# Optimization experiments

Hardware: AMD Instinct MI355X
Metric: run time of the kernel (lower is better)

The kernel has to match this reference:

```python
import jax, jax.numpy as jnp
import numpy as np
import math

N_HEAD = 12
BLOCK = 256  # local attention block size (ls)
EPS = 1e-6


def _rotate(x):
    # pairs (a, b) -> (-b, a) over last dim (matches rotate_embeddings)
    a = x[..., 0::2]
    b = x[..., 1::2]
    return jnp.stack([-b, a], axis=-1).reshape(x.shape)


def setup_inputs() -> dict:
    key = jax.random.key(0)
    k1, k2, k3 = jax.random.split(key, 3)
    B, T, C = 4, 8192, 768
    s = 0.02
    return {
        "x": jax.random.normal(k1, (B, T, C), jnp.float32),
        "w_qkv": jax.random.normal(k2, (C, 3 * C), jnp.float32) * s,
        "w_ln": jnp.ones((C,), jnp.float32),
        "w_proj": jax.random.normal(k3, (C, C), jnp.float32) * s,
    }


def reference(x, w_qkv, w_ln, w_proj):
    B, T, C = x.shape
    nh, ls = N_HEAD, BLOCK
    hd = C // nh
    ng = T // ls

    xb = x.reshape(B, ng, ls, C)
    qkv = xb @ w_qkv                                   # (B,ng,ls,3C)
    q, k, v = jnp.split(qkv, 3, axis=-1)

    # QK RMSNorm over full embedding dim (before head split)
    def rms(t):
        return t * jax.lax.rsqrt(jnp.mean(t * t, axis=-1, keepdims=True) + EPS) * w_ln
    q, k = rms(q), rms(k)

    # split heads: (B,ng,nh,ls,hd)
    def heads(t):
        return jnp.swapaxes(t.reshape(B, ng, ls, nh, hd), 2, 3)
    q, k, v = heads(q), heads(k), heads(v)

    # RoPE (repo layout: freqs tiled via cat((ts,ts)), interleaved pair rotation)
    pos = 10000.0 ** ((-2.0 * jnp.arange(0, hd, 2, dtype=jnp.float32) - 1.0) / hd)
    ts = jnp.arange(ls, dtype=jnp.float32)[:, None] * pos[None, :]   # (ls, hd/2)
    rot = jnp.concatenate([ts, ts], axis=-1)                          # (ls, hd)
    cos, sin = jnp.cos(rot), jnp.sin(rot)
    q = q * cos + _rotate(q) * sin
    k = k * cos + _rotate(k) * sin

    # block-causal scores: causal only within each local block
    scale = 1.0 / math.sqrt(hd)
    att = jnp.einsum('bgnqd,bgnkd->bgnqk', q, k) * scale              # (B,ng,nh,ls,ls)
    mask = jnp.tril(jnp.ones((ls, ls), dtype=bool))
    att = jnp.where(mask, att, -jnp.finfo(att.dtype).max)
    att = jax.nn.softmax(att, axis=-1)
    y = jnp.einsum('bgnqk,bgnkd->bgnqd', att, v)                      # (B,ng,nh,ls,hd)

    y = jnp.swapaxes(y, 2, 3).reshape(B, ng, ls, C)
    y = y @ w_proj
    return y.reshape(B, T, C)
```

## Files before the change

kernel.cpp:

```cpp
#include <hip/hip_runtime.h>
#include <math.h>

typedef __attribute__((ext_vector_type(8))) short bf16x8;
typedef __attribute__((ext_vector_type(4))) short bf16x4;
typedef __attribute__((ext_vector_type(2))) short bf16x2;
typedef __attribute__((ext_vector_type(4))) float f32x4;
typedef __attribute__((ext_vector_type(16))) float f32x16;

#define NH 12
#define HD 64
#define C0 768
#define C3 2304
#define LS 256
#define KT12 12

static __device__ __forceinline__ float bf2f(short u) {
  union { unsigned int i; float f; } c;
  c.i = ((unsigned int)(unsigned short)u) << 16;
  return c.f;
}
static __device__ __forceinline__ short f2bf(float f) {
  union { float f; unsigned int i; } c; c.f = f;
  unsigned int x = c.i;
  x += 0x7fffu + ((x >> 16) & 1u);
  return (short)(x >> 16);
}
static __device__ __forceinline__ unsigned pk2(float a, float b) {
  return (unsigned)(unsigned short)f2bf(a) | ((unsigned)(unsigned short)f2bf(b) << 16);
}

static __device__ __forceinline__ void gload_lds16(const short* g, const short* l) {
  unsigned long long ga = (unsigned long long)g;
  unsigned int la = (unsigned int)(unsigned long long)l;
  __builtin_amdgcn_global_load_lds(
      (const __attribute__((address_space(1))) void*)ga,
      (__attribute__((address_space(3))) void*)la, 16, 0, 0);
}

__global__ __launch_bounds__(256) void cast_pack_A_kernel(const float* __restrict__ x,
                                                          short* __restrict__ Apk) {
  __shared__ short sb[256 * 64];
  int bm = blockIdx.x, kt = blockIdx.y, t = threadIdx.x;
#pragma unroll
  for (int i = 0; i < 8; ++i) {
    int seg = i * 256 + t;
    int row = seg >> 3, sc8 = seg & 7;
    const float* src = x + ((long)(bm * 256 + row)) * C0 + kt * 64 + sc8 * 8;
    float4 v0 = *(const float4*)src;
    float4 v1 = *(const float4*)(src + 4);
    bf16x8 o = { f2bf(v0.x), f2bf(v0.y), f2bf(v0.z), f2bf(v0.w),
                 f2bf(v1.x), f2bf(v1.y), f2bf(v1.z), f2bf(v1.w) };
    *(bf16x8*)&sb[row * 64 + ((sc8 ^ (row & 7)) << 3)] = o;
  }
  __syncthreads();
#pragma unroll
  for (int i = 0; i < 8; ++i) {
    int c = i * 256 + t;
    int l = c & 63, f = c >> 6;
    int ks = f & 3, mt = (f >> 2) & 3, mh = f >> 4;
    int row = mh * 128 + mt * 32 + (l & 31);
    int kc = ks * 2 + (l >> 5);
    bf16x8 v = *(bf16x8*)&sb[row * 64 + ((kc ^ (row & 7)) << 3)];
    *(bf16x8*)&Apk[(((long)bm * KT12 + kt) * 2048 + c) * 8] = v;
  }
}

template <int WNG>
__global__ __launch_bounds__(256) void cast_pack_B_kernel(const float* __restrict__ w,
                                                          short* __restrict__ Bpk, int N) {
  __shared__ short sb[WNG * 64 * 64];
  int bn = blockIdx.x, kt = blockIdx.y, t = threadIdx.x;
#pragma unroll
  for (int i = 0; i < WNG * 2; ++i) {
    int seg = i * 256 + t;
    int k = seg / (WNG * 8);
    int nc = (seg % (WNG * 8)) * 8;
    const float* src = w + ((long)(kt * 64 + k)) * N + bn * (WNG * 64) + nc;
    float4 v0 = *(const float4*)src;
    float4 v1 = *(const float4*)(src + 4);
    sb[(nc + 0) * 64 + k] = f2bf(v0.x); sb[(nc + 1) * 64 + k] = f2bf(v0.y);
    sb[(nc + 2) * 64 + k] = f2bf(v0.z); sb[(nc + 3) * 64 + k] = f2bf(v0.w);
    sb[(nc + 4) * 64 + k] = f2bf(v1.x); sb[(nc + 5) * 64 + k] = f2bf(v1.y);
    sb[(nc + 6) * 64 + k] = f2bf(v1.z); sb[(nc + 7) * 64 + k] = f2bf(v1.w);
  }
  __syncthreads();
#pragma unroll
  for (int i = 0; i < WNG * 2; ++i) {
    int c = i * 256 + t;
    int l = c & 63, f = c >> 6;
    int ks = f & 3, nt = (f >> 2) & 1, wng = f >> 3;
    int col = wng * 64 + nt * 32 + (l & 31);
    int kk = ks * 16 + (l >> 5) * 8;
    bf16x8 v = *(bf16x8*)&sb[col * 64 + kk];
    *(bf16x8*)&Bpk[(((long)bn * KT12 + kt) * (WNG * 512) + c) * 8] = v;
  }
}

__global__ void rope_tab_kernel(float* __restrict__ cost, float* __restrict__ sint) {
  int t = blockIdx.x, d = threadIdx.x;
  int i = d & 31;
  float freq = powf(10000.0f, -(float)(4 * i + 1) / 64.0f);
  float th = (float)t * freq;
  cost[t * 64 + d] = cosf(th);
  sint[t * 64 + d] = sinf(th);
}

#define PH_OPEN                                        \
  __builtin_amdgcn_s_barrier();                        \
  asm volatile("s_waitcnt lgkmcnt(0)" ::: "memory");   \
  __builtin_amdgcn_sched_barrier(0);                   \
  __builtin_amdgcn_s_setprio(1);
#define PH_MID __builtin_amdgcn_s_setprio(0);
#define PH_CLOSE                                       \
  asm volatile("s_waitcnt vmcnt(2)" ::: "memory");     \
  __builtin_amdgcn_s_barrier();
#define MM8(ASET, BSET, MP, NT)                                                     \
  { _Pragma("unroll") for (int m2_ = 0; m2_ < 2; ++m2_)                             \
      _Pragma("unroll") for (int ks_ = 0; ks_ < 4; ++ks_)                           \
        acc[(MP)*2 + m2_][NT] = __builtin_amdgcn_mfma_f32_32x32x16_bf16(            \
            ASET[m2_ * 4 + ks_], BSET[ks_], acc[(MP)*2 + m2_][NT], 0, 0, 0); }

template <int OUT_F32>
__global__ __launch_bounds__(512, 2) void gemm32_kernel(const short* __restrict__ Apk,
                                                        const short* __restrict__ Bpk,
                                                        void* __restrict__ Cout,
                                                        int N, int K, int nbn) {
  __shared__ short lds[65536];
  int t = threadIdx.x, lane = t & 63, wave = t >> 6;
  int wm = (wave >> 2) * 128, wng = wave & 3, wn = wng * 64, mh = wave >> 2;
  int id = blockIdx.x;
  int cpx = gridDim.x >> 3;
  int sw = (id & 7) * cpx + (id >> 3);
  int bm = sw / nbn, bn = sw % nbn;

  f32x16 acc[4][2];
#pragma unroll
  for (int m = 0; m < 4; ++m)
#pragma unroll
    for (int n = 0; n < 2; ++n)
#pragma unroll
      for (int r = 0; r < 16; ++r) acc[m][n][r] = 0.f;

  bf16x8 a0[8], a1[8], b0[4], b1[4];

  auto STAGE = [&](int s) {
    if (s >= 4 * KT12) return;
    int q = s & 3, Ts = s >> 2;
    int bb = (Ts & 1) * 32768;
    if (q < 2) {
      int c = q * 1024 + t;
      const short* src = Apk + ((long)bm * KT12 + Ts) * 16384 + (long)c * 8;
      gload_lds16(src, &lds[bb + c * 8]);
      gload_lds16(src + 4096, &lds[bb + (c + 512) * 8]);
    } else {
      int c = (q - 2) * 1024 + t;
      const short* src = Bpk + ((long)bn * KT12 + Ts) * 16384 + (long)c * 8;
      gload_lds16(src, &lds[bb + 16384 + c * 8]);
      gload_lds16(src + 4096, &lds[bb + 16384 + (c + 512) * 8]);
    }
  };
  auto LDA = [&](bf16x8* d, int b, int mhalf) {
#pragma unroll
    for (int m2 = 0; m2 < 2; ++m2)
#pragma unroll
      for (int ks = 0; ks < 4; ++ks)
        d[m2 * 4 + ks] =
            *(bf16x8*)&lds[b * 32768 + ((mh * 16 + (mhalf * 2 + m2) * 4 + ks) * 64 + lane) * 8];
  };
  auto LDB = [&](bf16x8* d, int b, int nt) {
#pragma unroll
    for (int ks = 0; ks < 4; ++ks)
      d[ks] = *(bf16x8*)&lds[b * 32768 + 16384 + ((wng * 8 + nt * 4 + ks) * 64 + lane) * 8];
  };

  for (int s = 0; s < 7; ++s) STAGE(s);
  asm volatile("s_waitcnt vmcnt(6)" ::: "memory");
  __builtin_amdgcn_s_barrier();
  LDA(a0, 0, 0);
  LDB(b0, 0, 0);
  LDB(b1, 0, 1);

  for (int it = 0; it < KT12 / 2; ++it) {
    int P0 = 8 * it;
    PH_OPEN; MM8(a0, b0, 0, 0); PH_MID;
    LDA(a1, 0, 1); STAGE(P0 + 7); PH_CLOSE;
    PH_OPEN; MM8(a0, b1, 0, 1); PH_MID;
    LDA(a0, 1, 0); STAGE(P0 + 8); PH_CLOSE;
    PH_OPEN; MM8(a1, b0, 1, 0); PH_MID;
    LDB(b0, 1, 0); STAGE(P0 + 9); PH_CLOSE;
    PH_OPEN; MM8(a1, b1, 1, 1); PH_MID;
    LDB(b1, 1, 1); STAGE(P0 + 10); PH_CLOSE;
    PH_OPEN; MM8(a0, b0, 0, 0); PH_MID;
    LDA(a1, 1, 1); STAGE(P0 + 11); PH_CLOSE;
    PH_OPEN; MM8(a0, b1, 0, 1); PH_MID;
    LDA(a0, 0, 0); STAGE(P0 + 12); PH_CLOSE;
    PH_OPEN; MM8(a1, b0, 1, 0); PH_MID;
    LDB(b0, 0, 0); STAGE(P0 + 13); PH_CLOSE;
    PH_OPEN; MM8(a1, b1, 1, 1); PH_MID;
    LDB(b1, 0, 1); STAGE(P0 + 14); PH_CLOSE;
  }

  long crow0 = (long)bm * 256 + wm;
  long ccol0 = (long)bn * 256 + wn;
  int rbase = 4 * (lane >> 5);
  int cl = lane & 31;
#pragma unroll
  for (int mt = 0; mt < 4; ++mt)
#pragma unroll
    for (int nt = 0; nt < 2; ++nt)
#pragma unroll
      for (int reg = 0; reg < 16; ++reg) {
        long row = crow0 + mt * 32 + (reg & 3) + 8 * (reg >> 2) + rbase;
        long col = ccol0 + nt * 32 + cl;
        float v = acc[mt][nt][reg];
        if (OUT_F32) ((float*)Cout)[row * N + col] = v;
        else ((short*)Cout)[row * N + col] = f2bf(v);
      }
}

template <int OUT_F32>
__global__ __launch_bounds__(256, 2) void gemm128_kernel(const short* __restrict__ Arm,
                                                         const short* __restrict__ Bpk,
                                                         void* __restrict__ Cout,
                                                         int N, int K, int nbn) {
  __shared__ short lds[32768];
  int t = threadIdx.x, lane = t & 63, wave = t >> 6;
  int wm = (wave >> 1) * 64, wng = wave & 1;
  int id = blockIdx.x;
  int cpx = gridDim.x >> 3;
  int sw = (id & 7) * cpx + (id >> 3);
  int bm = sw / nbn, bn = sw % nbn;
  int l31 = lane & 31, lh = lane >> 5;

  f32x16 acc[2][2];
#pragma unroll
  for (int m = 0; m < 2; ++m)
#pragma unroll
    for (int n = 0; n < 2; ++n)
#pragma unroll
      for (int r = 0; r < 16; ++r) acc[m][n][r] = 0.f;

  auto STAGE = [&](int T) {
    int bb = (T & 1) * 16384;
#pragma unroll
    for (int i = 0; i < 4; ++i) {
      int q = i * 256 + t;
      int row = q >> 3, cp = q & 7;
      const short* ga = Arm + ((long)(bm * 128 + row)) * K + T * 64 + ((cp ^ (row & 7)) * 8);
      gload_lds16(ga, &lds[bb + q * 8]);
      const short* gb = Bpk + ((long)bn * KT12 + T) * 8192 + (long)q * 8;
      gload_lds16(gb, &lds[bb + 8192 + q * 8]);
    }
  };

  STAGE(0);
  asm volatile("s_waitcnt vmcnt(0)" ::: "memory");
  __builtin_amdgcn_s_barrier();

  for (int T = 0; T < KT12; ++T) {
    int bb = (T & 1) * 16384;
    if (T + 1 < KT12) STAGE(T + 1);
    bf16x8 a[2][4], b[2][4];
#pragma unroll
    for (int mt = 0; mt < 2; ++mt) {
      int row = wm + mt * 32 + l31;
      int s8 = row & 7;
#pragma unroll
      for (int ks = 0; ks < 4; ++ks) {
        int g = (ks * 2 + lh) ^ s8;
        a[mt][ks] = *(bf16x8*)&lds[bb + row * 64 + g * 8];
      }
    }
#pragma unroll
    for (int nt = 0; nt < 2; ++nt)
#pragma unroll
      for (int ks = 0; ks < 4; ++ks)
        b[nt][ks] = *(bf16x8*)&lds[bb + 8192 + (((wng * 2 + nt) * 4 + ks) * 64 + lane) * 8];
    __builtin_amdgcn_s_setprio(1);
#pragma unroll
    for (int mt = 0; mt < 2; ++mt)
#pragma unroll
      for (int nt = 0; nt < 2; ++nt)
#pragma unroll
        for (int ks = 0; ks < 4; ++ks)
          acc[mt][nt] = __builtin_amdgcn_mfma_f32_32x32x16_bf16(a[mt][ks], b[nt][ks],
                                                                acc[mt][nt], 0, 0, 0);
    __builtin_amdgcn_s_setprio(0);
    asm volatile("s_waitcnt lgkmcnt(0)" ::: "memory");
    asm volatile("s_waitcnt vmcnt(0)" ::: "memory");
    __builtin_amdgcn_s_barrier();
  }

  long crow0 = (long)bm * 128 + wm;
  long ccol0 = (long)bn * 128 + wng * 64;
  int rbase = 4 * lh;
#pragma unroll
  for (int mt = 0; mt < 2; ++mt)
#pragma unroll
    for (int nt = 0; nt < 2; ++nt)
#pragma unroll
      for (int reg = 0; reg < 16; ++reg) {
        long row = crow0 + mt * 32 + (reg & 3) + 8 * (reg >> 2) + rbase;
        long col = ccol0 + nt * 32 + l31;
        float v = acc[mt][nt][reg];
        if (OUT_F32) ((float*)Cout)[row * N + col] = v;
        else ((short*)Cout)[row * N + col] = f2bf(v);
      }
}

__global__ __launch_bounds__(384) void norm_rope_kernel(short* __restrict__ QKV,
    const float* __restrict__ w_ln, const float* __restrict__ cost,
    const float* __restrict__ sint) {
  int row = blockIdx.x;
  int t = row & 255;
  int i = threadIdx.x;
  bool isq = i < 192;
  int e0 = (i - (isq ? 0 : 192)) * 4;
  long off = (long)row * C3 + (isq ? 0 : C0) + e0;
  bf16x4 v4 = *(const bf16x4*)&QKV[off];
  float a = bf2f(v4.x), b = bf2f(v4.y), c = bf2f(v4.z), d = bf2f(v4.w);
  float ss = a * a + b * b + c * c + d * d;
#pragma unroll
  for (int o = 32; o > 0; o >>= 1) ss += __shfl_down(ss, o);
  __shared__ float red[6];
  if ((i & 63) == 0) red[i >> 6] = ss;
  __syncthreads();
  float s3 = isq ? (red[0] + red[1] + red[2]) : (red[3] + red[4] + red[5]);
  float r = rsqrtf(s3 * (1.0f / 768.0f) + 1e-6f);
  float4 wl = *(const float4*)&w_ln[e0];
  int d0 = e0 & 63;
  float4 cs = *(const float4*)&cost[t * 64 + d0];
  float4 sn = *(const float4*)&sint[t * 64 + d0];
  float n0 = a * r * wl.x, n1 = b * r * wl.y, n2 = c * r * wl.z, n3 = d * r * wl.w;
  bf16x4 o;
  o.x = f2bf(n0 * cs.x - n1 * sn.x);
  o.y = f2bf(n1 * cs.y + n0 * sn.y);
  o.z = f2bf(n2 * cs.z - n3 * sn.z);
  o.w = f2bf(n3 * cs.w + n2 * sn.w);
  *(bf16x4*)&QKV[off] = o;
}

__global__ __launch_bounds__(512, 3) void attn_kernel(const short* __restrict__ QKV,
                                                      short* __restrict__ Y) {
  __shared__ short Ks[256 * 64];
  __shared__ short Vt[64 * 256];
  int blk = blockIdx.x;
  int bg = blk / NH, h = blk % NH;
  const long base = (long)bg * LS * C3 + h * HD;
  int tid = threadIdx.x, lane = tid & 63, wave = tid >> 6;
  int lr = lane & 15, lg = lane >> 4;

#pragma unroll
  for (int it = 0; it < 4; ++it) {
    int q = it * 512 + tid;
    int row = q >> 3, cp = q & 7;
    int gcp = cp ^ (row & 7);
    gload_lds16(QKV + base + (long)row * C3 + C0 + gcp * 8, &Ks[q * 8]);
  }
#pragma unroll
  for (int it = 0; it < 4; ++it) {
    int e = tid * 8 + it * 4096;
    int k = e >> 6, n = e & 63;
    bf16x8 v = *(const bf16x8*)&QKV[base + (long)k * C3 + 2 * C0 + n];
#pragma unroll
    for (int j = 0; j < 8; ++j) {
      int nn = n + j;
      int key = (nn & 7) ^ (nn >> 3);
      Vt[nn * 256 + (((k >> 3) ^ key) << 3) + (k & 7)] = v[j];
    }
  }
  asm volatile("s_waitcnt vmcnt(0)" ::: "memory");
  __syncthreads();

  int addrA = (((lane >> 4) & 1) * 32 + lr) * 4;
  int addrB = addrA + 64;
  bool selhi = (lane & 32) != 0;

  for (int tt = 0; tt < 2; ++tt) {
    int tile = (tt == 0) ? wave : (15 - wave);
    int m0 = tile * 16;
    bf16x8 qf[2];
#pragma unroll
    for (int ks = 0; ks < 2; ++ks)
      qf[ks] = *(const bf16x8*)&QKV[base + (long)(m0 + lr) * C3 + ks * 32 + lg * 8];

    f32x4 zero4 = {0.f, 0.f, 0.f, 0.f};
    f32x4 accs[16];
#pragma unroll
    for (int n = 0; n < 16; ++n) accs[n] = zero4;

    __builtin_amdgcn_s_setprio(1);
#pragma unroll
    for (int n = 0; n < 16; ++n) {
      if (n <= tile) {
        int row = n * 16 + lr, sw = row & 7;
        bf16x8 k0 = *(bf16x8*)&Ks[row * 64 + ((lg ^ sw) << 3)];
        bf16x8 k1 = *(bf16x8*)&Ks[row * 64 + (((4 + lg) ^ sw) << 3)];
        accs[n] = __builtin_amdgcn_mfma_f32_16x16x32_bf16(k0, qf[0], accs[n], 0, 0, 0);
        accs[n] = __builtin_amdgcn_mfma_f32_16x16x32_bf16(k1, qf[1], accs[n], 0, 0, 0);
      }
    }
    __builtin_amdgcn_s_setprio(0);

    float tm[16];
#pragma unroll
    for (int n = 0; n < 16; ++n) {
      if (n <= tile) {
        if (n == tile) {
#pragma unroll
          for (int r = 0; r < 4; ++r)
            accs[n][r] = (lg * 4 + r <= lr) ? accs[n][r] : -1e30f;
        }
        float m01 = fmaxf(accs[n][0], accs[n][1]);
        float m23 = fmaxf(accs[n][2], accs[n][3]);
        tm[n] = fmaxf(m01, m23);
      } else {
        tm[n] = -1e30f;
      }
    }
#pragma unroll
    for (int st = 1; st < 16; st <<= 1)
#pragma unroll
      for (int j = 0; j < 16; j += 2 * st) tm[j] = fmaxf(tm[j], tm[j + st]);
    float mloc = tm[0];
    mloc = fmaxf(mloc, __shfl_xor(mloc, 16));
    mloc = fmaxf(mloc, __shfl_xor(mloc, 32));

    float ts[16];
#pragma unroll
    for (int n = 0; n < 16; ++n) {
      if (n <= tile) {
#pragma unroll
        for (int r = 0; r < 4; ++r) accs[n][r] = __expf((accs[n][r] - mloc) * 0.125f);
        float s01 = accs[n][0] + accs[n][1];
        float s23 = accs[n][2] + accs[n][3];
        ts[n] = s01 + s23;
      } else {
        ts[n] = 0.f;
      }
    }
#pragma unroll
    for (int st = 1; st < 16; st <<= 1)
#pragma unroll
      for (int j = 0; j < 16; j += 2 * st) ts[j] += ts[j + st];
    float s = ts[0];
    s += __shfl_xor(s, 16);
    s += __shfl_xor(s, 32);
    float rs = 1.0f / s;
    float rv[4];
#pragma unroll
    for (int r = 0; r < 4; ++r) {
      union { float f; int i; } c; c.f = rs;
      union { int i; float f; } o;
      o.i = __builtin_amdgcn_ds_bpermute((lg * 4 + r) * 4, c.i);
      rv[r] = o.f;
    }

    int ktmax = (m0 + 15) >> 5;
    f32x4 yacc[4];
#pragma unroll
    for (int n2 = 0; n2 < 4; ++n2) yacc[n2] = zero4;
#pragma unroll
    for (int kt = 0; kt < 8; ++kt) {
      if (kt <= ktmax) {
        int n0 = 2 * kt, n1 = 2 * kt + 1;
        unsigned a01_0 = pk2(accs[n0][0], accs[n0][1]);
        unsigned a23_0 = pk2(accs[n0][2], accs[n0][3]);
        unsigned a01_1 = (n1 <= tile) ? pk2(accs[n1][0], accs[n1][1]) : 0u;
        unsigned a23_1 = (n1 <= tile) ? pk2(accs[n1][2], accs[n1][3]) : 0u;
        union { unsigned u[4]; bf16x8 v; } af;
        unsigned g0a = (unsigned)__builtin_amdgcn_ds_bpermute(addrA, (int)a01_0);
        unsigned g0b = (unsigned)__builtin_amdgcn_ds_bpermute(addrA, (int)a01_1);
        unsigned g1a = (unsigned)__builtin_amdgcn_ds_bpermute(addrA, (int)a23_0);
        unsigned g1b = (unsigned)__builtin_amdgcn_ds_bpermute(addrA, (int)a23_1);
        unsigned g2a = (unsigned)__builtin_amdgcn_ds_bpermute(addrB, (int)a01_0);
        unsigned g2b = (unsigned)__builtin_amdgcn_ds_bpermute(addrB, (int)a01_1);
        unsigned g3a = (unsigned)__builtin_amdgcn_ds_bpermute(addrB, (int)a23_0);
        unsigned g3b = (unsigned)__builtin_amdgcn_ds_bpermute(addrB, (int)a23_1);
        af.u[0] = selhi ? g0b : g0a;
        af.u[1] = selhi ? g1b : g1a;
        af.u[2] = selhi ? g2b : g2a;
        af.u[3] = selhi ? g3b : g3a;
        int ac = kt * 32 + lg * 8;
        __builtin_amdgcn_s_setprio(1);
#pragma unroll
        for (int n2 = 0; n2 < 4; ++n2) {
          int vn = n2 * 16 + lr;
          int vkey = (vn & 7) ^ (vn >> 3);
          bf16x8 vb = *(bf16x8*)&Vt[vn * 256 + (((ac >> 3) ^ vkey) << 3)];
          yacc[n2] = __builtin_amdgcn_mfma_f32_16x16x32_bf16(af.v, vb, yacc[n2], 0, 0, 0);
        }
        __builtin_amdgcn_s_setprio(0);
      }
    }

#pragma unroll
    for (int n2 = 0; n2 < 4; ++n2) {
#pragma unroll
      for (int r = 0; r < 4; ++r) {
        int row = m0 + lg * 4 + r, d = n2 * 16 + lr;
        Y[((long)(bg * LS + row)) * C0 + h * HD + d] = f2bf(yacc[n2][r] * rv[r]);
      }
    }
  }
}

extern "C" void kernel_launch(void* const* d_in, const int* in_sizes, int n_in,
                              void* d_out, int out_size, void* d_ws, size_t ws_size,
                              hipStream_t stream) {
  (void)in_sizes; (void)n_in; (void)out_size; (void)ws_size;
  const float* x = (const float*)d_in[0];
  const float* w_qkv = (const float*)d_in[1];
  const float* w_ln = (const float*)d_in[2];
  const float* w_proj = (const float*)d_in[3];
  float* out = (float*)d_out;

  char* ws = (char*)d_ws;
  short* Apk     = (short*)(ws + 0);
  short* QKV     = (short*)(ws + 50331648);
  short* Yb      = (short*)(ws + 201326592);
  short* WqkvPk  = (short*)(ws + 251658240);
  short* WprojPk = (short*)(ws + 255197184);
  float* cost    = (float*)(ws + 256376832);
  float* sint    = (float*)(ws + 256442368);

  cast_pack_A_kernel<<<dim3(128, KT12), 256, 0, stream>>>(x, Apk);
  cast_pack_B_kernel<4><<<dim3(9, KT12), 256, 0, stream>>>(w_qkv, WqkvPk, C3);
  cast_pack_B_kernel<2><<<dim3(6, KT12), 256, 0, stream>>>(w_proj, WprojPk, C0);
  rope_tab_kernel<<<256, 64, 0, stream>>>(cost, sint);

  gemm32_kernel<0><<<128 * 9, 512, 0, stream>>>(Apk, WqkvPk, QKV, C3, C0, 9);
  norm_rope_kernel<<<32768, 384, 0, stream>>>(QKV, w_ln, cost, sint);
  attn_kernel<<<128 * NH, 512, 0, stream>>>(QKV, Yb);
  gemm128_kernel<1><<<256 * 6, 256, 0, stream>>>(Yb, WprojPk, out, C0, C0, 6);
}
```

Before: 362.9 us.

## Rework norm-rope to one wave per row, simplify V swizzle and softmax reductions

The norm/RoPE kernel now gives one 64-lane wave to each q or k row instead of a 384-thread block per token. This removes the LDS reduction and the __syncthreads, and uses wider vector loads. The attention kernel's V transpose loads 4 elements per thread with a simpler XOR swizzle, which changes the LDS bank-conflict pattern. The softmax max and sum reductions use four running accumulators instead of 16-entry tree arrays, to cut register pressure. The gemm32 kernel loses its output-type template and its unused K parameter.

```diff
diff --git a/kernel.cpp b/kernel.cpp
--- a/kernel.cpp
+++ b/kernel.cpp
@@ -120,11 +120,10 @@
         acc[(MP)*2 + m2_][NT] = __builtin_amdgcn_mfma_f32_32x32x16_bf16(            \
             ASET[m2_ * 4 + ks_], BSET[ks_], acc[(MP)*2 + m2_][NT], 0, 0, 0); }
 
-template <int OUT_F32>
 __global__ __launch_bounds__(512, 2) void gemm32_kernel(const short* __restrict__ Apk,
                                                         const short* __restrict__ Bpk,
-                                                        void* __restrict__ Cout,
-                                                        int N, int K, int nbn) {
+                                                        short* __restrict__ Cout,
+                                                        int N, int nbn) {
   __shared__ short lds[65536];
   int t = threadIdx.x, lane = t & 63, wave = t >> 6;
   int wm = (wave >> 2) * 128, wng = wave & 3, wn = wng * 64, mh = wave >> 2;
@@ -212,9 +211,7 @@
       for (int reg = 0; reg < 16; ++reg) {
         long row = crow0 + mt * 32 + (reg & 3) + 8 * (reg >> 2) + rbase;
         long col = ccol0 + nt * 32 + cl;
-        float v = acc[mt][nt][reg];
-        if (OUT_F32) ((float*)Cout)[row * N + col] = v;
-        else ((short*)Cout)[row * N + col] = f2bf(v);
+        Cout[row * N + col] = f2bf(acc[mt][nt][reg]);
       }
 }
 
@@ -308,36 +305,61 @@
       }
 }
 
-__global__ __launch_bounds__(384) void norm_rope_kernel(short* __restrict__ QKV,
+__global__ __launch_bounds__(512) void norm_rope_kernel(short* __restrict__ QKV,
     const float* __restrict__ w_ln, const float* __restrict__ cost,
     const float* __restrict__ sint) {
-  int row = blockIdx.x;
+  int wid = (blockIdx.x << 3) + (threadIdx.x >> 6);
+  int lane = threadIdx.x & 63;
+  int row = wid >> 1;
   int t = row & 255;
-  int i = threadIdx.x;
-  bool isq = i < 192;
-  int e0 = (i - (isq ? 0 : 192)) * 4;
-  long off = (long)row * C3 + (isq ? 0 : C0) + e0;
-  bf16x4 v4 = *(const bf16x4*)&QKV[off];
-  float a = bf2f(v4.x), b = bf2f(v4.y), c = bf2f(v4.z), d = bf2f(v4.w);
-  float ss = a * a + b * b + c * c + d * d;
-#pragma unroll
-  for (int o = 32; o > 0; o >>= 1) ss += __shfl_down(ss, o);
-  __shared__ float red[6];
-  if ((i & 63) == 0) red[i >> 6] = ss;
-  __syncthreads();
-  float s3 = isq ? (red[0] + red[1] + red[2]) : (red[3] + red[4] + red[5]);
-  float r = rsqrtf(s3 * (1.0f / 768.0f) + 1e-6f);
-  float4 wl = *(const float4*)&w_ln[e0];
-  int d0 = e0 & 63;
-  float4 cs = *(const float4*)&cost[t * 64 + d0];
-  float4 sn = *(const float4*)&sint[t * 64 + d0];
-  float n0 = a * r * wl.x, n1 = b * r * wl.y, n2 = c * r * wl.z, n3 = d * r * wl.w;
-  bf16x4 o;
-  o.x = f2bf(n0 * cs.x - n1 * sn.x);
-  o.y = f2bf(n1 * cs.y + n0 * sn.y);
-  o.z = f2bf(n2 * cs.z - n3 * sn.z);
-  o.w = f2bf(n3 * cs.w + n2 * sn.w);
-  *(bf16x4*)&QKV[off] = o;
+  long base = (long)row * C3 + (wid & 1) * C0;
+  int e8 = lane * 8, e4 = 512 + lane * 4;
+  bf16x8 v8 = *(const bf16x8*)&QKV[base + e8];
+  bf16x4 v4 = *(const bf16x4*)&QKV[base + e4];
+  float f[12];
+#pragma unroll
+  for (int j = 0; j < 8; ++j) f[j] = bf2f(v8[j]);
+#pragma unroll
+  for (int j = 0; j < 4; ++j) f[8 + j] = bf2f(v4[j]);
+  float ss = 0.f;
+#pragma unroll
+  for (int j = 0; j < 12; ++j) ss += f[j] * f[j];
+#pragma unroll
+  for (int o = 32; o > 0; o >>= 1) ss += __shfl_xor(ss, o);
+  float r = rsqrtf(ss * (1.0f / 768.0f) + 1e-6f);
+  float4 w0 = *(const float4*)&w_ln[e8];
+  float4 w1 = *(const float4*)&w_ln[e8 + 4];
+  float4 w2 = *(const float4*)&w_ln[e4];
+  float n[12];
+  n[0] = f[0] * r * w0.x;  n[1] = f[1] * r * w0.y;
+  n[2] = f[2] * r * w0.z;  n[3] = f[3] * r * w0.w;
+  n[4] = f[4] * r * w1.x;  n[5] = f[5] * r * w1.y;
+  n[6] = f[6] * r * w1.z;  n[7] = f[7] * r * w1.w;
+  n[8] = f[8] * r * w2.x;  n[9] = f[9] * r * w2.y;
+  n[10] = f[10] * r * w2.z; n[11] = f[11] * r * w2.w;
+  int d8 = e8 & 63, d4 = e4 & 63;
+  const float* cb = cost + t * 64;
+  const float* sbp = sint + t * 64;
+  float4 c0 = *(const float4*)&cb[d8], c1 = *(const float4*)&cb[d8 + 4];
+  float4 c2 = *(const float4*)&cb[d4];
+  float4 s0 = *(const float4*)&sbp[d8], s1 = *(const float4*)&sbp[d8 + 4];
+  float4 s2 = *(const float4*)&sbp[d4];
+  bf16x8 o8;
+  bf16x4 o4;
+  o8[0] = f2bf(n[0] * c0.x - n[1] * s0.x);
+  o8[1] = f2bf(n[1] * c0.y + n[0] * s0.y);
+  o8[2] = f2bf(n[2] * c0.z - n[3] * s0.z);
+  o8[3] = f2bf(n[3] * c0.w + n[2] * s0.w);
+  o8[4] = f2bf(n[4] * c1.x - n[5] * s1.x);
+  o8[5] = f2bf(n[5] * c1.y + n[4] * s1.y);
+  o8[6] = f2bf(n[6] * c1.z - n[7] * s1.z);
+  o8[7] = f2bf(n[7] * c1.w + n[6] * s1.w);
+  o4[0] = f2bf(n[8] * c2.x - n[9] * s2.x);
+  o4[1] = f2bf(n[9] * c2.y + n[8] * s2.y);
+  o4[2] = f2bf(n[10] * c2.z - n[11] * s2.z);
+  o4[3] = f2bf(n[11] * c2.w + n[10] * s2.w);
+  *(bf16x8*)&QKV[base + e8] = o8;
+  *(bf16x4*)&QKV[base + e4] = o4;
 }
 
 __global__ __launch_bounds__(512, 3) void attn_kernel(const short* __restrict__ QKV,
@@ -358,15 +380,14 @@
     gload_lds16(QKV + base + (long)row * C3 + C0 + gcp * 8, &Ks[q * 8]);
   }
 #pragma unroll
-  for (int it = 0; it < 4; ++it) {
-    int e = tid * 8 + it * 4096;
+  for (int it = 0; it < 8; ++it) {
+    int e = tid * 4 + it * 2048;
     int k = e >> 6, n = e & 63;
-    bf16x8 v = *(const bf16x8*)&QKV[base + (long)k * C3 + 2 * C0 + n];
-#pragma unroll
-    for (int j = 0; j < 8; ++j) {
+    bf16x4 v = *(const bf16x4*)&QKV[base + (long)k * C3 + 2 * C0 + n];
+#pragma unroll
+    for (int j = 0; j < 4; ++j) {
       int nn = n + j;
-      int key = (nn & 7) ^ (nn >> 3);
-      Vt[nn * 256 + (((k >> 3) ^ key) << 3) + (k & 7)] = v[j];
+      Vt[nn * 256 + (((k >> 3) ^ (nn & 7)) << 3) + (k & 7)] = v[j];
     }
   }
   asm volatile("s_waitcnt vmcnt(0)" ::: "memory");
@@ -402,7 +423,7 @@
     }
     __builtin_amdgcn_s_setprio(0);
 
-    float tm[16];
+    float q0 = -1e30f, q1 = -1e30f, q2 = -1e30f, q3 = -1e30f;
 #pragma unroll
     for (int n = 0; n < 16; ++n) {
       if (n <= tile) {
@@ -411,39 +432,37 @@
           for (int r = 0; r < 4; ++r)
             accs[n][r] = (lg * 4 + r <= lr) ? accs[n][r] : -1e30f;
         }
-        float m01 = fmaxf(accs[n][0], accs[n][1]);
-        float m23 = fmaxf(accs[n][2], accs[n][3]);
-        tm[n] = fmaxf(m01, m23);
-      } else {
-        tm[n] = -1e30f;
-      }
-    }
-#pragma unroll
-    for (int st = 1; st < 16; st <<= 1)
-#pragma unroll
-      for (int j = 0; j < 16; j += 2 * st) tm[j] = fmaxf(tm[j], tm[j + st]);
-    float mloc = tm[0];
+        float a01 = fmaxf(accs[n][0], accs[n][1]);
+        float a23 = fmaxf(accs[n][2], accs[n][3]);
+        float mn = fmaxf(a01, a23);
+        switch (n & 3) {
+          case 0: q0 = fmaxf(q0, mn); break;
+          case 1: q1 = fmaxf(q1, mn); break;
+          case 2: q2 = fmaxf(q2, mn); break;
+          default: q3 = fmaxf(q3, mn); break;
+        }
+      }
+    }
+    float mloc = fmaxf(fmaxf(q0, q1), fmaxf(q2, q3));
     mloc = fmaxf(mloc, __shfl_xor(mloc, 16));
     mloc = fmaxf(mloc, __shfl_xor(mloc, 32));
 
-    float ts[16];
+    float s0 = 0.f, s1 = 0.f, s2 = 0.f, s3 = 0.f;
 #pragma unroll
     for (int n = 0; n < 16; ++n) {
       if (n <= tile) {
 #pragma unroll
         for (int r = 0; r < 4; ++r) accs[n][r] = __expf((accs[n][r] - mloc) * 0.125f);
-        float s01 = accs[n][0] + accs[n][1];
-        float s23 = accs[n][2] + accs[n][3];
-        ts[n] = s01 + s23;
-      } else {
-        ts[n] = 0.f;
-      }
-    }
-#pragma unroll
-    for (int st = 1; st < 16; st <<= 1)
-#pragma unroll
-      for (int j = 0; j < 16; j += 2 * st) ts[j] += ts[j + st];
-    float s = ts[0];
+        float a = (accs[n][0] + accs[n][1]) + (accs[n][2] + accs[n][3]);
+        switch (n & 3) {
+          case 0: s0 += a; break;
+          case 1: s1 += a; break;
+          case 2: s2 += a; break;
+          default: s3 += a; break;
+        }
+      }
+    }
+    float s = (s0 + s1) + (s2 + s3);
     s += __shfl_xor(s, 16);
     s += __shfl_xor(s, 32);
     float rs = 1.0f / s;
@@ -486,8 +505,7 @@
 #pragma unroll
         for (int n2 = 0; n2 < 4; ++n2) {
           int vn = n2 * 16 + lr;
-          int vkey = (vn & 7) ^ (vn >> 3);
-          bf16x8 vb = *(bf16x8*)&Vt[vn * 256 + (((ac >> 3) ^ vkey) << 3)];
+          bf16x8 vb = *(bf16x8*)&Vt[vn * 256 + (((ac >> 3) ^ (vn & 7)) << 3)];
           yacc[n2] = __builtin_amdgcn_mfma_f32_16x16x32_bf16(af.v, vb, yacc[n2], 0, 0, 0);
         }
         __builtin_amdgcn_s_setprio(0);
@@ -529,8 +547,8 @@
   cast_pack_B_kernel<2><<<dim3(6, KT12), 256, 0, stream>>>(w_proj, WprojPk, C0);
   rope_tab_kernel<<<256, 64, 0, stream>>>(cost, sint);
 
-  gemm32_kernel<0><<<128 * 9, 512, 0, stream>>>(Apk, WqkvPk, QKV, C3, C0, 9);
-  norm_rope_kernel<<<32768, 384, 0, stream>>>(QKV, w_ln, cost, sint);
+  gemm32_kernel<<<128 * 9, 512, 0, stream>>>(Apk, WqkvPk, QKV, C3, 9);
+  norm_rope_kernel<<<8192, 512, 0, stream>>>(QKV, w_ln, cost, sint);
   attn_kernel<<<128 * NH, 512, 0, stream>>>(QKV, Yb);
   gemm128_kernel<1><<<256 * 6, 256, 0, stream>>>(Yb, WprojPk, out, C0, C0, 6);
 }
```

Measured after the change: 332.7 us. -8.3%, faster.
